# Kernel optimization log

Hardware: AMD Instinct MI355X
Metric: run time of the kernel (lower is better)

Reference implementation:

```python
import jax, jax.numpy as jnp
import numpy as np

B, N, D = 64, 256, 64          # datasets, samples per dataset, feature dim per variable (indim/2)
H, H2, OUT = 128, 64, 3        # hdlayers, hdlayers//2, outdim
REG, SIGMA, ALPHA = 1.0, 1.0, 2
BN_EPS = 1e-5


def _linear(k, fan_in, fan_out):
    kw, kb = jax.random.split(k)
    lim = 1.0 / np.sqrt(fan_in)
    w = jax.random.uniform(kw, (fan_in, fan_out), jnp.float32, -lim, lim)
    b = jax.random.uniform(kb, (fan_out,), jnp.float32, -lim, lim)
    return w, b


def setup_inputs() -> dict:
    key = jax.random.key(0)
    ks = jax.random.split(key, 10)
    w11_1, b11_1 = _linear(ks[2], D, H2)
    w11_2, b11_2 = _linear(ks[3], H2, H2)
    w12_1, b12_1 = _linear(ks[4], 2 * H2, H)
    w12_2, b12_2 = _linear(ks[5], H, H2)
    wc1, bc1 = _linear(ks[6], H2, OUT)
    w2, b2 = _linear(ks[7], OUT + 2, H2)
    wc2, bc2 = _linear(ks[8], H2, OUT)
    return {
        'x': jax.random.normal(ks[0], (B, N, D), jnp.float32),
        'y': jax.random.normal(ks[1], (B, N, D), jnp.float32),
        'w11_1': w11_1, 'b11_1': b11_1, 'w11_2': w11_2, 'b11_2': b11_2,
        'w12_1': w12_1, 'b12_1': b12_1, 'w12_2': w12_2, 'b12_2': b12_2,
        'wc1': wc1, 'bc1': bc1,
        'bn_gamma': jnp.ones((OUT + 2,), jnp.float32),
        'bn_beta': jnp.zeros((OUT + 2,), jnp.float32),
        'w2': w2, 'b2': b2, 'wc2': wc2, 'bc2': bc2,
    }


def _fro_normalize(t):
    # divide each [N, D] slice by its Frobenius norm
    return t / jnp.linalg.norm(t, axis=(1, 2), keepdims=True)


def _linear_regressor(x, y, reg):
    b, n, d = x.shape
    X = jnp.concatenate([jnp.ones((b, n, 1), x.dtype), x], axis=2)  # [B,N,d+1]
    P1 = jnp.einsum('bni,bnj->bij', X, X)                           # X^T X
    ridge = reg * jnp.eye(d + 1, dtype=x.dtype).at[0, 0].set(0.0)   # G^T G
    P2 = jnp.linalg.inv(P1 + ridge[None])
    P4 = X @ (P2 @ (jnp.swapaxes(X, 1, 2) @ y))
    loss = jnp.sum((y - P4) ** 2, axis=(1, 2))
    return loss, P4


def _gauss_kernel(x):
    # x: [B, N, F] -> [B, N, N]
    xn = jnp.sum(x * x, axis=-1)
    dist = xn[:, :, None] + xn[:, None, :] - 2.0 * jnp.einsum('bnd,bmd->bnm', x, x)
    return jnp.exp(-dist / SIGMA)


def _renyi_from_kernel(k):
    tr = jnp.trace(k, axis1=1, axis2=2)
    k = k / tr[:, None, None]
    ev = jnp.abs(jnp.linalg.eigvalsh(k))          # batched symeig eigenvalues
    return (1.0 / (1 - ALPHA)) * jnp.log2(jnp.sum(ev ** ALPHA, axis=-1))


def _renyi_mi(a, b):
    # batched normalized Renyi mutual information, a/b: [B, N, F]
    ka, kb = _gauss_kernel(a), _gauss_kernel(b)
    Hx = _renyi_from_kernel(ka)
    Hy = _renyi_from_kernel(kb)
    Hxy = _renyi_from_kernel(ka * kb)
    return (Hx + Hy - Hxy) / jnp.maximum(Hx, Hy)


def reference(x, y, w11_1, b11_1, w11_2, b11_2, w12_1, b12_1, w12_2, b12_2,
              wc1, bc1, bn_gamma, bn_beta, w2, b2, wc2, bc2):
    mlp11 = lambda t: jnp.maximum(t @ w11_1 + b11_1, 0.0) @ w11_2 + b11_2
    out_x = mlp11(x)                                  # [B,N,H2]
    out_y = mlp11(y)

    out_c = jnp.concatenate([out_x, out_y], axis=2)   # [B,N,2*H2]
    out_c = jnp.maximum(out_c @ w12_1 + b12_1, 0.0)
    out_c = jnp.maximum(out_c @ w12_2 + b12_2, 0.0)
    out_c = out_c.mean(axis=1)                        # [B,H2]
    out_c = out_c @ wc1 + bc1                         # [B,OUT]
    prob1 = jax.nn.softmax(out_c, axis=1)

    out_xn = _fro_normalize(out_x)
    out_yn = _fro_normalize(out_y)
    xx = _fro_normalize(x)
    yy = _fro_normalize(y)

    rx, px = _linear_regressor(out_xn, yy, REG)       # predict y from f(x)
    ry, py = _linear_regressor(out_yn, xx, REG)       # predict x from f(y)

    ex = _renyi_mi(yy - px, x)                        # [B]
    ey = _renyi_mi(xx - py, y)

    rxy = jnp.stack([ex, ey], axis=1)                 # [B,2]
    in_c = jnp.concatenate([out_c, rxy], axis=1)      # [B,OUT+2]
    mu = in_c.mean(axis=0)
    var = in_c.var(axis=0)                            # biased, as in torch BN training
    in_c = (in_c - mu) / jnp.sqrt(var + BN_EPS) * bn_gamma + bn_beta
    in_c = jnp.maximum(in_c @ w2 + b2, 0.0)
    out_c_f = in_c @ wc2 + bc2
    prob2 = jax.nn.softmax(out_c_f, axis=1)

    return (out_c, rx, ry, ex, ey, out_c_f, prob1, prob2)
```

## Files before the change

### kernel.cpp

```cpp
#include <hip/hip_runtime.h>
#include <math.h>

#define NB 64
#define NS 256
#define ND 64
#define NH2 64
#define NH 128
#define WSTRIDE 4224


#define F4E(v_, e_) ((e_)==0?(v_).x:((e_)==1?(v_).y:((e_)==2?(v_).z:(v_).w)))

typedef __attribute__((ext_vector_type(8))) short bf16x8;
typedef __attribute__((ext_vector_type(4))) float f32x4;

__device__ __forceinline__ unsigned short f2bf(float f){
    union { float f; unsigned int u; } v; v.f = f;
    unsigned int r = v.u + 0x7fffu + ((v.u >> 16) & 1u);
    return (unsigned short)(r >> 16);
}
__device__ __forceinline__ float bf2f(unsigned short h){
    union { unsigned int u; float f; } v; v.u = ((unsigned int)h) << 16;
    return v.f;
}
__device__ __forceinline__ void sw2(unsigned short* ph, unsigned short* pl, int idx, float f){
    unsigned short h = f2bf(f);
    ph[idx] = h;
    pl[idx] = f2bf(f - bf2f(h));
}
__device__ __forceinline__ void sw2x2(unsigned short* ph, unsigned short* pl, int idx, float f0, float f1){
    unsigned short h0 = f2bf(f0), h1 = f2bf(f1);
    ushort2 hh; hh.x = h0; hh.y = h1;
    *(ushort2*)(ph + idx) = hh;
    ushort2 ll; ll.x = f2bf(f0 - bf2f(h0)); ll.y = f2bf(f1 - bf2f(h1));
    *(ushort2*)(pl + idx) = ll;
}

#define LD8(P_, row_, kb_) (*(const bf16x8*)((const char*)(P_) + (size_t)(row_)*144 + (kb_)))

__device__ __forceinline__ f32x4 mm64(
    const unsigned short* Ah, const unsigned short* Al,
    const unsigned short* Bh, const unsigned short* Bl,
    int ar, int br, int lrow, int lkb, f32x4 acc)
{
    const int ra = ar + lrow, rb = br + lrow;
    bf16x8 ah0 = LD8(Ah, ra, lkb), ah1 = LD8(Ah, ra, lkb+64);
    bf16x8 al0 = LD8(Al, ra, lkb), al1 = LD8(Al, ra, lkb+64);
    bf16x8 bh0 = LD8(Bh, rb, lkb), bh1 = LD8(Bh, rb, lkb+64);
    bf16x8 bl0 = LD8(Bl, rb, lkb), bl1 = LD8(Bl, rb, lkb+64);
    acc = __builtin_amdgcn_mfma_f32_16x16x32_bf16(ah0, bh0, acc, 0,0,0);
    acc = __builtin_amdgcn_mfma_f32_16x16x32_bf16(ah1, bh1, acc, 0,0,0);
    acc = __builtin_amdgcn_mfma_f32_16x16x32_bf16(ah0, bl0, acc, 0,0,0);
    acc = __builtin_amdgcn_mfma_f32_16x16x32_bf16(ah1, bl1, acc, 0,0,0);
    acc = __builtin_amdgcn_mfma_f32_16x16x32_bf16(al0, bh0, acc, 0,0,0);
    acc = __builtin_amdgcn_mfma_f32_16x16x32_bf16(al1, bh1, acc, 0,0,0);
    return acc;
}

__global__ __launch_bounds__(512) void k1_fused(
    const float* __restrict__ x, const float* __restrict__ y,
    const float* __restrict__ w11_1, const float* __restrict__ b11_1,
    const float* __restrict__ w11_2, const float* __restrict__ b11_2,
    const float* __restrict__ w12_1, const float* __restrict__ b12_1,
    const float* __restrict__ w12_2, const float* __restrict__ b12_2,
    float* __restrict__ out_x, float* __restrict__ out_y,
    float* __restrict__ mean_part)
{
    const int b = blockIdx.x >> 2, tile = blockIdx.x & 3;
    const int t = threadIdx.x;
    const int lane = t & 63, wv = t >> 6;
    const int lrow = lane & 15;
    const int lkb  = (lane >> 4) * 16;
    const int row0g = b*NS + tile*64;

    __shared__ unsigned short XYh[9216], XYl[9216];
    __shared__ unsigned short W1h[4608], W1l[4608];
    __shared__ unsigned short W2h[4608], W2l[4608];
    __shared__ unsigned short Hh [9216], Hl [9216];
    __shared__ unsigned short Oh [9216], Ol [9216];
    __shared__ float msum[8*68];

    #pragma unroll
    for (int u=0;u<4;u++){
        int id = t + 512*u;
        int r = id>>4, c0 = (id&15)*4;
        const float* src = (r < 64) ? (x + ((size_t)(row0g + r))*ND)
                                    : (y + ((size_t)(row0g + r - 64))*ND);
        float4 v = *(const float4*)(src + c0);
        sw2x2(XYh, XYl, r*72 + c0,   v.x, v.y);
        sw2x2(XYh, XYl, r*72 + c0+2, v.z, v.w);
    }
    {
        int rp = t>>4, c0 = (t&15)*4;
        float4 a0 = *(const float4*)(w11_1 + (size_t)(2*rp  )*64 + c0);
        float4 a1 = *(const float4*)(w11_1 + (size_t)(2*rp+1)*64 + c0);
        float4 b0 = *(const float4*)(w11_2 + (size_t)(2*rp  )*64 + c0);
        float4 b1 = *(const float4*)(w11_2 + (size_t)(2*rp+1)*64 + c0);
        #pragma unroll
        for (int i2=0;i2<4;i2++){
            sw2x2(W1h, W1l, (c0+i2)*72 + 2*rp, F4E(a0,i2), F4E(a1,i2));
            sw2x2(W2h, W2l, (c0+i2)*72 + 2*rp, F4E(b0,i2), F4E(b1,i2));
        }
    }
    __syncthreads();

    {
        const int ar = 16*wv;
        #pragma unroll
        for (int jt=0; jt<4; jt++){
            float bb = b11_1[jt*16 + lrow];
            f32x4 acc = {bb,bb,bb,bb};
            acc = mm64(XYh, XYl, W1h, W1l, ar, jt*16, lrow, lkb, acc);
            #pragma unroll
            for (int e=0;e<4;e++){
                int row = ar + (lane>>4)*4 + e;
                int col = jt*16 + lrow;
                sw2(Hh, Hl, row*72 + col, fmaxf(acc[e], 0.f));
            }
        }
    }
    __syncthreads();

    #pragma unroll
    for (int u=0;u<2;u++){
        int id = t + 512*u;
        int krp = id>>5, c0 = (id&31)*4;
        float4 v0 = *(const float4*)(w12_1 + (size_t)(2*krp  )*NH + c0);
        float4 v1 = *(const float4*)(w12_1 + (size_t)(2*krp+1)*NH + c0);
        #pragma unroll
        for (int i2=0;i2<4;i2++)
            sw2x2(XYh, XYl, (c0+i2)*72 + 2*krp, F4E(v0,i2), F4E(v1,i2));
    }
    {
        const int ar = 16*wv;
        #pragma unroll
        for (int jt=0; jt<4; jt++){
            float bb = b11_2[jt*16 + lrow];
            f32x4 acc = {bb,bb,bb,bb};
            acc = mm64(Hh, Hl, W2h, W2l, ar, jt*16, lrow, lkb, acc);
            #pragma unroll
            for (int e=0;e<4;e++){
                int row = ar + (lane>>4)*4 + e;
                int col = jt*16 + lrow;
                float v = acc[e];
                sw2(Oh, Ol, row*72 + col, v);
                float* dst = (row < 64) ? out_x : out_y;
                dst[((size_t)(row0g + (row & 63)))*NH2 + col] = v;
            }
        }
    }
    __syncthreads();

    const int rt = wv & 3, cq = wv >> 2;
    f32x4 acc3[4];
    #pragma unroll
    for (int q=0; q<4; q++){
        float bb = b12_1[(4*cq+q)*16 + lrow];
        f32x4 v = {bb,bb,bb,bb};
        acc3[q] = v;
    }
    #pragma unroll
    for (int q=0; q<4; q++)
        acc3[q] = mm64(Oh, Ol, XYh, XYl, 16*rt, 16*(4*cq+q), lrow, lkb, acc3[q]);
    __syncthreads();

    #pragma unroll
    for (int u=0;u<2;u++){
        int id = t + 512*u;
        int krp = id>>5, c0 = (id&31)*4;
        float4 v0 = *(const float4*)(w12_1 + (size_t)(64+2*krp  )*NH + c0);
        float4 v1 = *(const float4*)(w12_1 + (size_t)(64+2*krp+1)*NH + c0);
        #pragma unroll
        for (int i2=0;i2<4;i2++)
            sw2x2(XYh, XYl, (c0+i2)*72 + 2*krp, F4E(v0,i2), F4E(v1,i2));
    }
    {
        int krp = t>>4, c0 = (t&15)*4;
        float4 h0a = *(const float4*)(w12_2 + (size_t)(2*krp  )*NH2 + c0);
        float4 h0b = *(const float4*)(w12_2 + (size_t)(2*krp+1)*NH2 + c0);
        float4 h1a = *(const float4*)(w12_2 + (size_t)(64+2*krp  )*NH2 + c0);
        float4 h1b = *(const float4*)(w12_2 + (size_t)(64+2*krp+1)*NH2 + c0);
        #pragma unroll
        for (int i2=0;i2<4;i2++){
            sw2x2(W2h, W2l, (c0+i2)*72 + 2*krp, F4E(h0a,i2), F4E(h0b,i2));
            sw2x2(W1h, W1l, (c0+i2)*72 + 2*krp, F4E(h1a,i2), F4E(h1b,i2));
        }
    }
    __syncthreads();

    #pragma unroll
    for (int q=0; q<4; q++)
        acc3[q] = mm64(Oh, Ol, XYh, XYl, 64 + 16*rt, 16*(4*cq+q), lrow, lkb, acc3[q]);
    #pragma unroll
    for (int q=0; q<4; q++){
        #pragma unroll
        for (int e=0;e<4;e++){
            int row = 16*rt + (lane>>4)*4 + e;
            int col = 16*(4*cq+q) + lrow;
            float v = fmaxf(acc3[q][e], 0.f);
            int idx = (col < 64) ? (row*72 + col) : ((64+row)*72 + (col-64));
            sw2(Hh, Hl, idx, v);
        }
    }
    __syncthreads();

    {
        f32x4 acc2[2];
        #pragma unroll
        for (int q=0; q<2; q++){
            const int jc = 2*cq + q;
            float bb = b12_2[jc*16 + lrow];
            f32x4 v = {bb,bb,bb,bb};
            acc2[q] = v;
            acc2[q] = mm64(Hh, Hl, W2h, W2l, 16*rt,      16*jc, lrow, lkb, acc2[q]);
            acc2[q] = mm64(Hh, Hl, W1h, W1l, 64 + 16*rt, 16*jc, lrow, lkb, acc2[q]);
        }
        #pragma unroll
        for (int q=0; q<2; q++){
            const int jc = 2*cq + q;
            float s = fmaxf(acc2[q][0],0.f) + fmaxf(acc2[q][1],0.f)
                    + fmaxf(acc2[q][2],0.f) + fmaxf(acc2[q][3],0.f);
            s += __shfl_down(s, 32);
            s += __shfl_down(s, 16);
            if (lane < 16) msum[wv*68 + jc*16 + lane] = s;
        }
    }
    __syncthreads();
    if (t < 64){
        const int w0 = (t>>5)*4;
        float ss = msum[(w0+0)*68 + t] + msum[(w0+1)*68 + t]
                 + msum[(w0+2)*68 + t] + msum[(w0+3)*68 + t];
        mean_part[((size_t)(b*4+tile))*64 + t] = ss;
    }
}

__global__ __launch_bounds__(256) void k2ab(
    const float* __restrict__ fx, const float* __restrict__ fy,
    const float* __restrict__ x, const float* __restrict__ y,
    float* __restrict__ wbuf)
{
    const int bs = blockIdx.x;
    const int side = bs & 1, b = bs >> 1;
    const float* feat = side ? fy : fx;
    const float* targ = side ? x : y;
    float* wb = wbuf + (size_t)bs*WSTRIDE;
    const int t = threadIdx.x;
    const int lane = t & 63, wv = t >> 6;
    const int lrow = lane & 15;
    const int lkb  = (lane >> 4) * 16;
    const float inv256 = 1.0f/256.0f;

    __shared__ float Wf[64*68];
    __shared__ float Rf[64*68];
    __shared__ unsigned short Zh[4608], Zl[4608], Th[4608], Tl[4608];
    __shared__ unsigned short Eh[4608], El[4608];
    __shared__ unsigned short Wth[2][4608], Wtl[2][4608];
    __shared__ float cspA[16*68], cspB[16*68];
    __shared__ float szs[64], sts[64];
    __shared__ float sc[8], red4[4];

    {
        float szp0=0.f,szp1=0.f,szp2=0.f,szp3=0.f;
        float stp0=0.f,stp1=0.f,stp2=0.f,stp3=0.f;
        float tsq=0.f;
        for (int c=0;c<4;c++){
            #pragma unroll
            for (int u=0;u<4;u++){
                int id = t + 256*u;
                int r = id>>4, c0 = (id&15)*4;
                float4 v = *(const float4*)(feat + ((size_t)(b*NS + c*64 + r))*NH2 + c0);
                float4 w = *(const float4*)(targ + ((size_t)(b*NS + c*64 + r))*ND + c0);
                szp0+=v.x; szp1+=v.y; szp2+=v.z; szp3+=v.w;
                stp0+=w.x; stp1+=w.y; stp2+=w.z; stp3+=w.w;
                tsq += w.x*w.x + w.y*w.y + w.z*w.z + w.w*w.w;
            }
        }
        const int g2 = t>>4, c0 = (t&15)*4;
        cspA[g2*68 + c0+0] = szp0; cspA[g2*68 + c0+1] = szp1;
        cspA[g2*68 + c0+2] = szp2; cspA[g2*68 + c0+3] = szp3;
        cspB[g2*68 + c0+0] = stp0; cspB[g2*68 + c0+1] = stp1;
        cspB[g2*68 + c0+2] = stp2; cspB[g2*68 + c0+3] = stp3;
        float tq = tsq;
        #pragma unroll
        for (int off=32; off; off>>=1) tq += __shfl_down(tq, off);
        if (lane==0) red4[wv] = tq;
    }
    __syncthreads();
    if (t < 64){
        float sa=0.f, sb=0.f;
        #pragma unroll
        for (int g2=0; g2<16; g2++){ sa += cspA[g2*68+t]; sb += cspB[g2*68+t]; }
        szs[t] = sa; sts[t] = sb;
        float s2 = sa*sa;
        #pragma unroll
        for (int off=32; off; off>>=1) s2 += __shfl_down(s2, off);
        if (t==0) sc[2] = s2;
    }
    if (t==0) sc[1] = red4[0]+red4[1]+red4[2]+red4[3];
    __syncthreads();

    f32x4 accA[4], accR[4];
    #pragma unroll
    for (int jt=0;jt<4;jt++){
        f32x4 z = {0.f,0.f,0.f,0.f};
        accA[jt]=z; accR[jt]=z;
    }
    for (int c=0;c<4;c++){
        if (c) __syncthreads();
        #pragma unroll
        for (int u=0;u<4;u++){
            int id = t + 256*u;
            int r = id>>4, c0 = (id&15)*4;
            float4 v = *(const float4*)(feat + ((size_t)(b*NS + c*64 + r))*NH2 + c0);
            float4 w = *(const float4*)(targ + ((size_t)(b*NS + c*64 + r))*ND + c0);
            v.x -= szs[c0+0]*inv256; v.y -= szs[c0+1]*inv256;
            v.z -= szs[c0+2]*inv256; v.w -= szs[c0+3]*inv256;
            sw2(Zh,Zl,(c0+0)*72+r, v.x); sw2(Zh,Zl,(c0+1)*72+r, v.y);
            sw2(Zh,Zl,(c0+2)*72+r, v.z); sw2(Zh,Zl,(c0+3)*72+r, v.w);
            sw2(Th,Tl,(c0+0)*72+r, w.x); sw2(Th,Tl,(c0+1)*72+r, w.y);
            sw2(Th,Tl,(c0+2)*72+r, w.z); sw2(Th,Tl,(c0+3)*72+r, w.w);
        }
        __syncthreads();
        #pragma unroll
        for (int jt=0;jt<4;jt++){
            accA[jt] = mm64(Zh,Zl,Zh,Zl, 16*wv, 16*jt, lrow, lkb, accA[jt]);
            accR[jt] = mm64(Zh,Zl,Th,Tl, 16*wv, 16*jt, lrow, lkb, accR[jt]);
        }
    }
    {
        const int gi0 = 16*wv + (lane>>4)*4;
        #pragma unroll
        for (int jt=0;jt<4;jt++){
            #pragma unroll
            for (int e=0;e<4;e++){
                Wf[(gi0+e)*68 + 16*jt + lrow] = accA[jt][e];
                Rf[(gi0+e)*68 + 16*jt + lrow] = accR[jt][e];
            }
        }
    }
    __syncthreads();
    if (t<64){
        float dg = Wf[t*68+t];
        #pragma unroll
        for (int off=32; off; off>>=1) dg += __shfl_down(dg, off);
        if (t==0){
            float zn2 = dg + sc[2]*inv256;
            sc[0] = 1.0f/sqrtf(zn2);
            sc[1] = 1.0f/sqrtf(sc[1]);
        }
    }
    __syncthreads();
    const float zinv = sc[0], tinv = sc[1];
    const float z2 = zinv*zinv, zt = zinv*tinv;
    const float i23 = 2.0f/3.0f, i13 = 1.0f/3.0f;
    const int i = t>>2, qd = t&3;
    {
        #pragma unroll
        for (int q=0;q<4;q++){
            const int j = qd*16 + q*4;
            float4 a4 = *(const float4*)(Wf + i*68 + j);
            float e0 = i23*z2*a4.x - ((i==j  ) ? i13 : 0.f);
            float e1 = i23*z2*a4.y - ((i==j+1) ? i13 : 0.f);
            float e2 = i23*z2*a4.z - ((i==j+2) ? i13 : 0.f);
            float e3 = i23*z2*a4.w - ((i==j+3) ? i13 : 0.f);
            sw2x2(Eh, El, i*72 + j,   e0, e1);
            sw2x2(Eh, El, i*72 + j+2, e2, e3);
            float4 rv = *(float4*)(Rf + i*68 + j);
            float r0 = i23*zt*rv.x;
            float r1 = i23*zt*rv.y;
            float r2 = i23*zt*rv.z;
            float r3 = i23*zt*rv.w;
            *(float4*)(Rf + i*68 + j) = make_float4(r0,r1,r2,r3);
            sw2(Wth[0], Wtl[0], (j  )*72 + i, r0);
            sw2(Wth[0], Wtl[0], (j+1)*72 + i, r1);
            sw2(Wth[0], Wtl[0], (j+2)*72 + i, r2);
            sw2(Wth[0], Wtl[0], (j+3)*72 + i, r3);
        }
    }
    __syncthreads();

    int cur = 0;
    for (int n=0; n<12; n++){
        f32x4 acc[4];
        #pragma unroll
        for (int jt=0; jt<4; jt++){
            f32x4 zz = {0.f,0.f,0.f,0.f};
            acc[jt] = mm64(Eh, El, Wth[cur], Wtl[cur], 16*wv, jt*16, lrow, lkb, zz);
        }
        const int gi0 = 16*wv + (lane>>4)*4;
        #pragma unroll
        for (int jt=0; jt<4; jt++){
            const int gj = jt*16 + lrow;
            float w0 = Rf[(gi0  )*68 + gj] - acc[jt][0];
            float w1 = Rf[(gi0+1)*68 + gj] - acc[jt][1];
            float w2 = Rf[(gi0+2)*68 + gj] - acc[jt][2];
            float w3 = Rf[(gi0+3)*68 + gj] - acc[jt][3];
            sw2x2(Wth[cur^1], Wtl[cur^1], gj*72 + gi0,   w0, w1);
            sw2x2(Wth[cur^1], Wtl[cur^1], gj*72 + gi0+2, w2, w3);
            if (n == 11){
                Wf[(gi0  )*68 + gj] = w0;  wb[(gi0  )*64 + gj] = w0;
                Wf[(gi0+1)*68 + gj] = w1;  wb[(gi0+1)*64 + gj] = w1;
                Wf[(gi0+2)*68 + gj] = w2;  wb[(gi0+2)*64 + gj] = w2;
                Wf[(gi0+3)*68 + gj] = w3;  wb[(gi0+3)*64 + gj] = w3;
            }
        }
        cur ^= 1;
        __syncthreads();
    }

    if (t < 64){
        float s = 0.f;
        for (int i2=0; i2<64; i2++) s += szs[i2]*Wf[i2*68 + t];
        wb[4096+t] = (tinv*sts[t] - zinv*s) * inv256;
    }
    if (t==0){ wb[4160] = zinv; wb[4161] = tinv; }
}

__global__ __launch_bounds__(512) void kRG(
    const float* __restrict__ fx, const float* __restrict__ fy,
    const float* __restrict__ x, const float* __restrict__ y,
    const float* __restrict__ wbuf,
    float* __restrict__ part3, float* __restrict__ dout)
{
    const int blk = blockIdx.x;
    const int jh = blk & 1;
    const int b = (blk >> 1) & (NB-1);
    const int side = (blk >> 1) >> 6;
    const float* feat = side ? fy : fx;
    const float* targ = side ? x : y;
    const float* bmat = side ? y : x;
    const float* wb = wbuf + (size_t)(b*2+side)*WSTRIDE;
    const int t = threadIdx.x;
    const int lane = t & 63, wv = t >> 6;
    const int lrow = lane & 15, lkb = (lane>>4)*16;

    __shared__ unsigned short resA[256*72];
    __shared__ unsigned short tgB [256*72];
    __shared__ unsigned short Zh[2*4608], Zl[2*4608];
    __shared__ unsigned short Wth[4608], Wtl[4608];
    __shared__ float c0s[64];
    __shared__ float nAs[256], nBs[256];
    __shared__ float red[8][3];
    __shared__ float lred[8];

    #pragma unroll
    for (int u=0;u<2;u++){
        int id = t + 512*u;
        int k = id>>4, c0 = (id&15)*4;
        float4 v = *(const float4*)(wb + (size_t)k*64 + c0);
        sw2(Wth, Wtl, (c0+0)*72 + k, v.x);
        sw2(Wth, Wtl, (c0+1)*72 + k, v.y);
        sw2(Wth, Wtl, (c0+2)*72 + k, v.z);
        sw2(Wth, Wtl, (c0+3)*72 + k, v.w);
    }
    if (t<64) c0s[t] = wb[4096+t];
    const float zinv = wb[4160], tinv = wb[4161];
    #pragma unroll
    for (int u=0;u<8;u++){
        int id = t + 512*u;
        int r = id>>4, c0 = (id&15)*4;
        float4 v = *(const float4*)(bmat + ((size_t)(b*NS+r))*ND + c0);
        ushort4 h;
        h.x=f2bf(v.x); h.y=f2bf(v.y); h.z=f2bf(v.z); h.w=f2bf(v.w);
        *(ushort4*)(tgB + r*72 + c0) = h;
    }
    #pragma unroll
    for (int u=0;u<2;u++){
        int id = t + 512*u;
        int r = id>>4, c0 = (id&15)*4;
        float4 v = *(const float4*)(feat + ((size_t)(b*NS + r))*NH2 + c0);
        sw2x2(Zh, Zl, r*72+c0,   v.x, v.y);
        sw2x2(Zh, Zl, r*72+c0+2, v.z, v.w);
    }
    __syncthreads();

    const int rt = wv & 3, cq = wv >> 2;
    float lacc = 0.f;
    for (int c=0; c<4; c++){
        if (c < 3){
            unsigned short* zh = Zh + ((c+1)&1)*4608;
            unsigned short* zl = Zl + ((c+1)&1)*4608;
            #pragma unroll
            for (int u=0;u<2;u++){
                int id = t + 512*u;
                int r = id>>4, c0 = (id&15)*4;
                float4 v = *(const float4*)(feat + ((size_t)(b*NS + (c+1)*64 + r))*NH2 + c0);
                sw2x2(zh, zl, r*72+c0,   v.x, v.y);
                sw2x2(zh, zl, r*72+c0+2, v.z, v.w);
            }
        }
        const unsigned short* zh = Zh + (c&1)*4608;
        const unsigned short* zl = Zl + (c&1)*4608;
        f32x4 acc[2];
        #pragma unroll
        for (int q=0; q<2; q++){
            f32x4 zz = {0.f,0.f,0.f,0.f};
            acc[q] = mm64(zh, zl, Wth, Wtl, 16*rt, 16*(2*cq+q), lrow, lkb, zz);
        }
        const int r0 = 16*rt + (lane>>4)*4;
        #pragma unroll
        for (int q=0; q<2; q++){
            const int gj = 16*(2*cq+q) + lrow;
            const float cc = c0s[gj];
            #pragma unroll
            for (int e=0;e<4;e++){
                const int grow = c*64 + r0 + e;
                float qv = targ[((size_t)(b*NS+grow))*ND + gj];
                float rr = tinv*qv - zinv*acc[q][e] - cc;
                lacc += rr*rr;
                resA[grow*72 + gj] = f2bf(rr);
            }
        }
        __syncthreads();
    }

    {
        float l = lacc;
        #pragma unroll
        for (int off=32; off; off>>=1) l += __shfl_down(l, off);
        if (lane==0) lred[wv] = l;
    }
    if (t < 256){
        float sa=0.f, sb=0.f;
        #pragma unroll
        for (int j8=0;j8<8;j8++){
            bf16x8 va = *(const bf16x8*)((const char*)resA + (size_t)t*144 + j8*16);
            bf16x8 vb = *(const bf16x8*)((const char*)tgB  + (size_t)t*144 + j8*16);
            #pragma unroll
            for (int e2=0;e2<8;e2++){
                float fa = bf2f((unsigned short)va[e2]);
                float fb = bf2f((unsigned short)vb[e2]);
                sa += fa*fa; sb += fb*fb;
            }
        }
        nAs[t] = sa; nBs[t] = sb;
    }
    __syncthreads();
    if (t==0 && jh==0){
        float ls = 0.f;
        #pragma unroll
        for (int w=0;w<8;w++) ls += lred[w];
        dout[(side?256:192)+b] = ls;
    }

    const char* pA = (const char*)resA;
    const char* pB = (const char*)tgB;
    const f32x4 zero4 = {0.f, 0.f, 0.f, 0.f};
    const float CEXP = -2.8853900817779268f;

    float Sa=0.f, Sb=0.f, Sab=0.f;
    #pragma unroll
    for (int it=0; it<2; it++){
        const int i0 = wv*32 + it*16;
        const int arow = i0 + lrow;
        bf16x8 aA0 = *(const bf16x8*)(pA + arow*144 + lkb);
        bf16x8 aA1 = *(const bf16x8*)(pA + arow*144 + lkb + 64);
        bf16x8 aB0 = *(const bf16x8*)(pB + arow*144 + lkb);
        bf16x8 aB1 = *(const bf16x8*)(pB + arow*144 + lkb + 64);
        float nAi[4], nBi[4];
        #pragma unroll
        for (int e=0;e<4;e++){
            int gi = i0 + (lane>>4)*4 + e;
            nAi[e] = nAs[gi]; nBi[e] = nBs[gi];
        }
        #pragma unroll
        for (int jt=0; jt<8; jt++){
            const int j0 = jh*128 + jt*16;
            const int brow = j0 + lrow;
            bf16x8 bA0 = *(const bf16x8*)(pA + brow*144 + lkb);
            bf16x8 bA1 = *(const bf16x8*)(pA + brow*144 + lkb + 64);
            bf16x8 bB0 = *(const bf16x8*)(pB + brow*144 + lkb);
            bf16x8 bB1 = *(const bf16x8*)(pB + brow*144 + lkb + 64);
            f32x4 cA = __builtin_amdgcn_mfma_f32_16x16x32_bf16(aA0, bA0, zero4, 0, 0, 0);
            cA = __builtin_amdgcn_mfma_f32_16x16x32_bf16(aA1, bA1, cA, 0, 0, 0);
            f32x4 cB = __builtin_amdgcn_mfma_f32_16x16x32_bf16(aB0, bB0, zero4, 0, 0, 0);
            cB = __builtin_amdgcn_mfma_f32_16x16x32_bf16(aB1, bB1, cB, 0, 0, 0);
            const int gj = j0 + lrow;
            const float nAj = nAs[gj], nBj = nBs[gj];
            #pragma unroll
            for (int e=0;e<4;e++){
                const int gi = i0 + (lane>>4)*4 + e;
                const float dda = (gi==gj) ? 0.f : (nAi[e] + nAj - 2.f*cA[e]);
                const float ddb = (gi==gj) ? 0.f : (nBi[e] + nBj - 2.f*cB[e]);
                const float ka2 = exp2f(CEXP*dda);
                const float kb2 = exp2f(CEXP*ddb);
                Sa += ka2; Sb += kb2; Sab += ka2*kb2;
            }
        }
    }
    #pragma unroll
    for (int off=32; off; off>>=1){
        Sa += __shfl_down(Sa,off); Sb += __shfl_down(Sb,off); Sab += __shfl_down(Sab,off);
    }
    if (lane==0){ red[wv][0]=Sa; red[wv][1]=Sb; red[wv][2]=Sab; }
    __syncthreads();
    if (t==0){
        float s0=0.f, s1=0.f, s2=0.f;
        #pragma unroll
        for (int w=0;w<8;w++){ s0 += red[w][0]; s1 += red[w][1]; s2 += red[w][2]; }
        float* o = part3 + (size_t)blk*3;
        o[0] = s0; o[1] = s1; o[2] = s2;
    }
}

__global__ __launch_bounds__(64) void k4_final(
    const float* __restrict__ mean_part, const float* __restrict__ part3,
    const float* __restrict__ wc1, const float* __restrict__ bc1,
    const float* __restrict__ bn_gamma, const float* __restrict__ bn_beta,
    const float* __restrict__ w2, const float* __restrict__ b2,
    const float* __restrict__ wc2, const float* __restrict__ bc2,
    float* __restrict__ dout)
{
    const int t = threadIdx.x;
    __shared__ float ic[64][5];
    __shared__ float mu[5], iv[5];

    float o0 = bc1[0], o1 = bc1[1], o2 = bc1[2];
    for (int c=0;c<64;c++){
        float mv = mean_part[(t*4+0)*64+c] + mean_part[(t*4+1)*64+c]
                 + mean_part[(t*4+2)*64+c] + mean_part[(t*4+3)*64+c];
        mv *= (1.0f/256.0f);
        o0 += mv*wc1[c*3+0]; o1 += mv*wc1[c*3+1]; o2 += mv*wc1[c*3+2];
    }
    dout[t*3+0]=o0; dout[t*3+1]=o1; dout[t*3+2]=o2;
    {
        float m = fmaxf(o0,fmaxf(o1,o2));
        float e0=__expf(o0-m), e1=__expf(o1-m), e2=__expf(o2-m);
        float inv = 1.f/(e0+e1+e2);
        dout[640+t*3+0]=e0*inv; dout[640+t*3+1]=e1*inv; dout[640+t*3+2]=e2*inv;
    }
    float exy[2];
    #pragma unroll
    for (int side=0; side<2; side++){
        const float* pp = part3 + (size_t)((side*NB + t)*2)*3;
        float Sa = pp[0]+pp[3];
        float Sb = pp[1]+pp[4];
        float Sab= pp[2]+pp[5];
        float Hx  = 16.f - log2f(Sa);
        float Hy  = 16.f - log2f(Sb);
        float Hxy = 16.f - log2f(Sab);
        float mi = (Hx + Hy - Hxy) / fmaxf(Hx, Hy);
        dout[(side?384:320)+t] = mi;
        exy[side] = mi;
    }
    ic[t][0]=o0; ic[t][1]=o1; ic[t][2]=o2; ic[t][3]=exy[0]; ic[t][4]=exy[1];
    __syncthreads();
    if (t<5){
        float m=0.f;
        for (int bb=0;bb<64;bb++) m += ic[bb][t];
        m *= (1.f/64.f);
        float v=0.f;
        for (int bb=0;bb<64;bb++){ float d=ic[bb][t]-m; v+=d*d; }
        v *= (1.f/64.f);
        mu[t]=m; iv[t]=1.f/sqrtf(v+1e-5f);
    }
    __syncthreads();
    float vn[5];
    #pragma unroll
    for (int c=0;c<5;c++) vn[c] = (ic[t][c]-mu[c])*iv[c]*bn_gamma[c]+bn_beta[c];
    float q0=bc2[0], q1=bc2[1], q2=bc2[2];
    for (int j=0;j<64;j++){
        float hh = b2[j];
        #pragma unroll
        for (int c=0;c<5;c++) hh += vn[c]*w2[c*64+j];
        hh = fmaxf(hh,0.f);
        q0 += hh*wc2[j*3+0]; q1 += hh*wc2[j*3+1]; q2 += hh*wc2[j*3+2];
    }
    dout[448+t*3+0]=q0; dout[448+t*3+1]=q1; dout[448+t*3+2]=q2;
    float m = fmaxf(q0,fmaxf(q1,q2));
    float e0=__expf(q0-m), e1=__expf(q1-m), e2=__expf(q2-m);
    float inv=1.f/(e0+e1+e2);
    dout[832+t*3+0]=e0*inv; dout[832+t*3+1]=e1*inv; dout[832+t*3+2]=e2*inv;
}

extern "C" void kernel_launch(void* const* d_in, const int* in_sizes, int n_in,
                              void* d_out, int out_size, void* d_ws, size_t ws_size,
                              hipStream_t stream)
{
    const float* x     = (const float*)d_in[0];
    const float* y     = (const float*)d_in[1];
    const float* w11_1 = (const float*)d_in[2];
    const float* b11_1 = (const float*)d_in[3];
    const float* w11_2 = (const float*)d_in[4];
    const float* b11_2 = (const float*)d_in[5];
    const float* w12_1 = (const float*)d_in[6];
    const float* b12_1 = (const float*)d_in[7];
    const float* w12_2 = (const float*)d_in[8];
    const float* b12_2 = (const float*)d_in[9];
    const float* wc1   = (const float*)d_in[10];
    const float* bc1   = (const float*)d_in[11];
    const float* bn_g  = (const float*)d_in[12];
    const float* bn_b  = (const float*)d_in[13];
    const float* w2    = (const float*)d_in[14];
    const float* b2    = (const float*)d_in[15];
    const float* wc2   = (const float*)d_in[16];
    const float* bc2   = (const float*)d_in[17];

    float* ws   = (float*)d_ws;
    float* dout = (float*)d_out;
    float* out_x = ws;
    float* out_y = ws + 1048576;
    float* mean_part = ws + 2097152;
    float* part3 = mean_part + 16384;
    float* wbuf  = part3 + 3840;

    hipLaunchKernelGGL(k1_fused, dim3(NB*4), dim3(512), 0, stream,
        x,y,w11_1,b11_1,w11_2,b11_2,w12_1,b12_1,w12_2,b12_2,
        out_x,out_y,mean_part);
    hipLaunchKernelGGL(k2ab, dim3(2*NB), dim3(256), 0, stream,
        out_x,out_y,x,y,wbuf);
    hipLaunchKernelGGL(kRG, dim3(NB*2*2), dim3(512), 0, stream,
        out_x,out_y,x,y,wbuf,part3,dout);
    hipLaunchKernelGGL(k4_final, dim3(1), dim3(64), 0, stream,
        mean_part,part3,wc1,bc1,bn_g,bn_b,w2,b2,wc2,bc2,dout);
}
```

Measured before the change: 77.17 us.

## Double block size to 1024 threads in k1_fused and kRG, halving per-wave work

```diff
diff --git a/kernel.cpp b/kernel.cpp
--- a/kernel.cpp
+++ b/kernel.cpp
@@ -57,7 +57,7 @@
     return acc;
 }
 
-__global__ __launch_bounds__(512) void k1_fused(
+__global__ __launch_bounds__(1024) void k1_fused(
     const float* __restrict__ x, const float* __restrict__ y,
     const float* __restrict__ w11_1, const float* __restrict__ b11_1,
     const float* __restrict__ w11_2, const float* __restrict__ b11_2,
@@ -78,11 +78,11 @@
     __shared__ unsigned short W2h[4608], W2l[4608];
     __shared__ unsigned short Hh [9216], Hl [9216];
     __shared__ unsigned short Oh [9216], Ol [9216];
-    __shared__ float msum[8*68];
-
-    #pragma unroll
-    for (int u=0;u<4;u++){
-        int id = t + 512*u;
+    __shared__ float msum[16*68];
+
+    #pragma unroll
+    for (int u=0;u<2;u++){
+        int id = t + 1024*u;
         int r = id>>4, c0 = (id&15)*4;
         const float* src = (r < 64) ? (x + ((size_t)(row0g + r))*ND)
                                     : (y + ((size_t)(row0g + r - 64))*ND);
@@ -90,7 +90,7 @@
         sw2x2(XYh, XYl, r*72 + c0,   v.x, v.y);
         sw2x2(XYh, XYl, r*72 + c0+2, v.z, v.w);
     }
-    {
+    if (t < 512){
         int rp = t>>4, c0 = (t&15)*4;
         float4 a0 = *(const float4*)(w11_1 + (size_t)(2*rp  )*64 + c0);
         float4 a1 = *(const float4*)(w11_1 + (size_t)(2*rp+1)*64 + c0);
@@ -104,10 +104,12 @@
     }
     __syncthreads();
 
-    {
-        const int ar = 16*wv;
-        #pragma unroll
-        for (int jt=0; jt<4; jt++){
+    const int rtA = wv >> 1, cpA = wv & 1;
+    {
+        const int ar = 16*rtA;
+        #pragma unroll
+        for (int q=0; q<2; q++){
+            const int jt = 2*cpA + q;
             float bb = b11_1[jt*16 + lrow];
             f32x4 acc = {bb,bb,bb,bb};
             acc = mm64(XYh, XYl, W1h, W1l, ar, jt*16, lrow, lkb, acc);
@@ -121,10 +123,8 @@
     }
     __syncthreads();
 
-    #pragma unroll
-    for (int u=0;u<2;u++){
-        int id = t + 512*u;
-        int krp = id>>5, c0 = (id&31)*4;
+    {
+        int krp = t>>5, c0 = (t&31)*4;
         float4 v0 = *(const float4*)(w12_1 + (size_t)(2*krp  )*NH + c0);
         float4 v1 = *(const float4*)(w12_1 + (size_t)(2*krp+1)*NH + c0);
         #pragma unroll
@@ -132,9 +132,10 @@
             sw2x2(XYh, XYl, (c0+i2)*72 + 2*krp, F4E(v0,i2), F4E(v1,i2));
     }
     {
-        const int ar = 16*wv;
-        #pragma unroll
-        for (int jt=0; jt<4; jt++){
+        const int ar = 16*rtA;
+        #pragma unroll
+        for (int q=0; q<2; q++){
+            const int jt = 2*cpA + q;
             float bb = b11_2[jt*16 + lrow];
             f32x4 acc = {bb,bb,bb,bb};
             acc = mm64(Hh, Hl, W2h, W2l, ar, jt*16, lrow, lkb, acc);
@@ -152,29 +153,26 @@
     __syncthreads();
 
     const int rt = wv & 3, cq = wv >> 2;
-    f32x4 acc3[4];
-    #pragma unroll
-    for (int q=0; q<4; q++){
-        float bb = b12_1[(4*cq+q)*16 + lrow];
+    f32x4 acc3[2];
+    #pragma unroll
+    for (int q=0; q<2; q++){
+        const int jt = 2*cq + q;
+        float bb = b12_1[jt*16 + lrow];
         f32x4 v = {bb,bb,bb,bb};
         acc3[q] = v;
-    }
-    #pragma unroll
-    for (int q=0; q<4; q++)
-        acc3[q] = mm64(Oh, Ol, XYh, XYl, 16*rt, 16*(4*cq+q), lrow, lkb, acc3[q]);
-    __syncthreads();
-
-    #pragma unroll
-    for (int u=0;u<2;u++){
-        int id = t + 512*u;
-        int krp = id>>5, c0 = (id&31)*4;
+        acc3[q] = mm64(Oh, Ol, XYh, XYl, 16*rt, 16*jt, lrow, lkb, acc3[q]);
+    }
+    __syncthreads();
+
+    {
+        int krp = t>>5, c0 = (t&31)*4;
         float4 v0 = *(const float4*)(w12_1 + (size_t)(64+2*krp  )*NH + c0);
         float4 v1 = *(const float4*)(w12_1 + (size_t)(64+2*krp+1)*NH + c0);
         #pragma unroll
         for (int i2=0;i2<4;i2++)
             sw2x2(XYh, XYl, (c0+i2)*72 + 2*krp, F4E(v0,i2), F4E(v1,i2));
     }
-    {
+    if (t < 512){
         int krp = t>>4, c0 = (t&15)*4;
         float4 h0a = *(const float4*)(w12_2 + (size_t)(2*krp  )*NH2 + c0);
         float4 h0b = *(const float4*)(w12_2 + (size_t)(2*krp+1)*NH2 + c0);
@@ -189,14 +187,15 @@
     __syncthreads();
 
     #pragma unroll
-    for (int q=0; q<4; q++)
-        acc3[q] = mm64(Oh, Ol, XYh, XYl, 64 + 16*rt, 16*(4*cq+q), lrow, lkb, acc3[q]);
-    #pragma unroll
-    for (int q=0; q<4; q++){
+    for (int q=0; q<2; q++)
+        acc3[q] = mm64(Oh, Ol, XYh, XYl, 64 + 16*rt, 16*(2*cq+q), lrow, lkb, acc3[q]);
+    #pragma unroll
+    for (int q=0; q<2; q++){
+        const int jt = 2*cq + q;
         #pragma unroll
         for (int e=0;e<4;e++){
             int row = 16*rt + (lane>>4)*4 + e;
-            int col = 16*(4*cq+q) + lrow;
+            int col = 16*jt + lrow;
             float v = fmaxf(acc3[q][e], 0.f);
             int idx = (col < 64) ? (row*72 + col) : ((64+row)*72 + (col-64));
             sw2(Hh, Hl, idx, v);
@@ -205,29 +204,20 @@
     __syncthreads();
 
     {
-        f32x4 acc2[2];
-        #pragma unroll
-        for (int q=0; q<2; q++){
-            const int jc = 2*cq + q;
-            float bb = b12_2[jc*16 + lrow];
-            f32x4 v = {bb,bb,bb,bb};
-            acc2[q] = v;
-            acc2[q] = mm64(Hh, Hl, W2h, W2l, 16*rt,      16*jc, lrow, lkb, acc2[q]);
-            acc2[q] = mm64(Hh, Hl, W1h, W1l, 64 + 16*rt, 16*jc, lrow, lkb, acc2[q]);
-        }
-        #pragma unroll
-        for (int q=0; q<2; q++){
-            const int jc = 2*cq + q;
-            float s = fmaxf(acc2[q][0],0.f) + fmaxf(acc2[q][1],0.f)
-                    + fmaxf(acc2[q][2],0.f) + fmaxf(acc2[q][3],0.f);
-            s += __shfl_down(s, 32);
-            s += __shfl_down(s, 16);
-            if (lane < 16) msum[wv*68 + jc*16 + lane] = s;
-        }
+        const int jc = cq;
+        float bb = b12_2[jc*16 + lrow];
+        f32x4 acc2 = {bb,bb,bb,bb};
+        acc2 = mm64(Hh, Hl, W2h, W2l, 16*rt,      16*jc, lrow, lkb, acc2);
+        acc2 = mm64(Hh, Hl, W1h, W1l, 64 + 16*rt, 16*jc, lrow, lkb, acc2);
+        float s = fmaxf(acc2[0],0.f) + fmaxf(acc2[1],0.f)
+                + fmaxf(acc2[2],0.f) + fmaxf(acc2[3],0.f);
+        s += __shfl_down(s, 32);
+        s += __shfl_down(s, 16);
+        if (lane < 16) msum[wv*68 + jc*16 + lane] = s;
     }
     __syncthreads();
     if (t < 64){
-        const int w0 = (t>>5)*4;
+        const int w0 = (t>>4)*4;
         float ss = msum[(w0+0)*68 + t] + msum[(w0+1)*68 + t]
                  + msum[(w0+2)*68 + t] + msum[(w0+3)*68 + t];
         mean_part[((size_t)(b*4+tile))*64 + t] = ss;
@@ -416,7 +406,7 @@
     if (t==0){ wb[4160] = zinv; wb[4161] = tinv; }
 }
 
-__global__ __launch_bounds__(512) void kRG(
+__global__ __launch_bounds__(1024) void kRG(
     const float* __restrict__ fx, const float* __restrict__ fy,
     const float* __restrict__ x, const float* __restrict__ y,
     const float* __restrict__ wbuf,
@@ -440,13 +430,11 @@
     __shared__ unsigned short Wth[4608], Wtl[4608];
     __shared__ float c0s[64];
     __shared__ float nAs[256], nBs[256];
-    __shared__ float red[8][3];
-    __shared__ float lred[8];
-
-    #pragma unroll
-    for (int u=0;u<2;u++){
-        int id = t + 512*u;
-        int k = id>>4, c0 = (id&15)*4;
+    __shared__ float red[16][3];
+    __shared__ float lred[16];
+
+    {
+        int k = t>>4, c0 = (t&15)*4;
         float4 v = *(const float4*)(wb + (size_t)k*64 + c0);
         sw2(Wth, Wtl, (c0+0)*72 + k, v.x);
         sw2(Wth, Wtl, (c0+1)*72 + k, v.y);
@@ -456,60 +444,47 @@
     if (t<64) c0s[t] = wb[4096+t];
     const float zinv = wb[4160], tinv = wb[4161];
     #pragma unroll
-    for (int u=0;u<8;u++){
-        int id = t + 512*u;
+    for (int u=0;u<4;u++){
+        int id = t + 1024*u;
         int r = id>>4, c0 = (id&15)*4;
         float4 v = *(const float4*)(bmat + ((size_t)(b*NS+r))*ND + c0);
         ushort4 h;
         h.x=f2bf(v.x); h.y=f2bf(v.y); h.z=f2bf(v.z); h.w=f2bf(v.w);
         *(ushort4*)(tgB + r*72 + c0) = h;
     }
-    #pragma unroll
-    for (int u=0;u<2;u++){
-        int id = t + 512*u;
-        int r = id>>4, c0 = (id&15)*4;
+    {
+        int r = t>>4, c0 = (t&15)*4;
         float4 v = *(const float4*)(feat + ((size_t)(b*NS + r))*NH2 + c0);
         sw2x2(Zh, Zl, r*72+c0,   v.x, v.y);
         sw2x2(Zh, Zl, r*72+c0+2, v.z, v.w);
     }
     __syncthreads();
 
-    const int rt = wv & 3, cq = wv >> 2;
+    const int rt = wv & 3, ct = wv >> 2;
     float lacc = 0.f;
     for (int c=0; c<4; c++){
         if (c < 3){
             unsigned short* zh = Zh + ((c+1)&1)*4608;
             unsigned short* zl = Zl + ((c+1)&1)*4608;
-            #pragma unroll
-            for (int u=0;u<2;u++){
-                int id = t + 512*u;
-                int r = id>>4, c0 = (id&15)*4;
-                float4 v = *(const float4*)(feat + ((size_t)(b*NS + (c+1)*64 + r))*NH2 + c0);
-                sw2x2(zh, zl, r*72+c0,   v.x, v.y);
-                sw2x2(zh, zl, r*72+c0+2, v.z, v.w);
-            }
+            int r = t>>4, c0 = (t&15)*4;
+            float4 v = *(const float4*)(feat + ((size_t)(b*NS + (c+1)*64 + r))*NH2 + c0);
+            sw2x2(zh, zl, r*72+c0,   v.x, v.y);
+            sw2x2(zh, zl, r*72+c0+2, v.z, v.w);
         }
         const unsigned short* zh = Zh + (c&1)*4608;
         const unsigned short* zl = Zl + (c&1)*4608;
-        f32x4 acc[2];
-        #pragma unroll
-        for (int q=0; q<2; q++){
-            f32x4 zz = {0.f,0.f,0.f,0.f};
-            acc[q] = mm64(zh, zl, Wth, Wtl, 16*rt, 16*(2*cq+q), lrow, lkb, zz);
-        }
+        f32x4 zz = {0.f,0.f,0.f,0.f};
+        f32x4 acc = mm64(zh, zl, Wth, Wtl, 16*rt, 16*ct, lrow, lkb, zz);
         const int r0 = 16*rt + (lane>>4)*4;
-        #pragma unroll
-        for (int q=0; q<2; q++){
-            const int gj = 16*(2*cq+q) + lrow;
-            const float cc = c0s[gj];
-            #pragma unroll
-            for (int e=0;e<4;e++){
-                const int grow = c*64 + r0 + e;
-                float qv = targ[((size_t)(b*NS+grow))*ND + gj];
-                float rr = tinv*qv - zinv*acc[q][e] - cc;
-                lacc += rr*rr;
-                resA[grow*72 + gj] = f2bf(rr);
-            }
+        const int gj = 16*ct + lrow;
+        const float cc = c0s[gj];
+        #pragma unroll
+        for (int e=0;e<4;e++){
+            const int grow = c*64 + r0 + e;
+            float qv = targ[((size_t)(b*NS+grow))*ND + gj];
+            float rr = tinv*qv - zinv*acc[e] - cc;
+            lacc += rr*rr;
+            resA[grow*72 + gj] = f2bf(rr);
         }
         __syncthreads();
     }
@@ -539,7 +514,7 @@
     if (t==0 && jh==0){
         float ls = 0.f;
         #pragma unroll
-        for (int w=0;w<8;w++) ls += lred[w];
+        for (int w=0;w<16;w++) ls += lred[w];
         dout[(side?256:192)+b] = ls;
     }
 
@@ -549,9 +524,8 @@
     const float CEXP = -2.8853900817779268f;
 
     float Sa=0.f, Sb=0.f, Sab=0.f;
-    #pragma unroll
-    for (int it=0; it<2; it++){
-        const int i0 = wv*32 + it*16;
+    {
+        const int i0 = wv*16;
         const int arow = i0 + lrow;
         bf16x8 aA0 = *(const bf16x8*)(pA + arow*144 + lkb);
         bf16x8 aA1 = *(const bf16x8*)(pA + arow*144 + lkb + 64);
@@ -597,7 +571,7 @@
     if (t==0){
         float s0=0.f, s1=0.f, s2=0.f;
         #pragma unroll
-        for (int w=0;w<8;w++){ s0 += red[w][0]; s1 += red[w][1]; s2 += red[w][2]; }
+        for (int w=0;w<16;w++){ s0 += red[w][0]; s1 += red[w][1]; s2 += red[w][2]; }
         float* o = part3 + (size_t)blk*3;
         o[0] = s0; o[1] = s1; o[2] = s2;
     }
@@ -704,12 +678,12 @@
     float* part3 = mean_part + 16384;
     float* wbuf  = part3 + 3840;
 
-    hipLaunchKernelGGL(k1_fused, dim3(NB*4), dim3(512), 0, stream,
+    hipLaunchKernelGGL(k1_fused, dim3(NB*4), dim3(1024), 0, stream,
         x,y,w11_1,b11_1,w11_2,b11_2,w12_1,b12_1,w12_2,b12_2,
         out_x,out_y,mean_part);
     hipLaunchKernelGGL(k2ab, dim3(2*NB), dim3(256), 0, stream,
         out_x,out_y,x,y,wbuf);
-    hipLaunchKernelGGL(kRG, dim3(NB*2*2), dim3(512), 0, stream,
+    hipLaunchKernelGGL(kRG, dim3(NB*2*2), dim3(1024), 0, stream,
         out_x,out_y,x,y,wbuf,part3,dout);
     hipLaunchKernelGGL(k4_final, dim3(1), dim3(64), 0, stream,
         mean_part,part3,wc1,bc1,bn_g,bn_b,w2,b2,wc2,bc2,dout);
```

After: 76.81 us. No clear change (-0.5%).
